# Kernel optimization log

Hardware: AMD Instinct MI355X
Metric: run time of the kernel (lower is better)

The kernel has to match this reference:

```python
import jax, jax.numpy as jnp
import numpy as np

N_NODES = 50000
N_EDGES = 800000
EDGE_DIM = 64
HID = 64


def setup_inputs() -> dict:
    key = jax.random.key(0)
    ks = jax.random.split(key, 8)
    hidden_atom_emb = jax.random.normal(ks[0], (N_NODES, HID), dtype=jnp.float32)
    edge_emb = jax.random.normal(ks[1], (N_EDGES, EDGE_DIM), dtype=jnp.float32)
    edge_list = jax.random.randint(ks[2], (N_EDGES, 2), 0, N_NODES, dtype=jnp.int64)
    # filter MLP params (xavier-uniform-like scaling)
    lim1 = float(np.sqrt(6.0 / (EDGE_DIM + HID)))
    W1 = jax.random.uniform(ks[3], (EDGE_DIM, HID), minval=-lim1, maxval=lim1, dtype=jnp.float32)
    b1 = jnp.zeros((HID,), dtype=jnp.float32)
    lim2 = float(np.sqrt(6.0 / (HID + HID)))
    W2 = jax.random.uniform(ks[4], (HID, HID), minval=-lim2, maxval=lim2, dtype=jnp.float32)
    b2 = jnp.zeros((HID,), dtype=jnp.float32)
    lim3 = 1.414 * float(np.sqrt(6.0 / (HID + 1)))
    linear_coef = jax.random.uniform(ks[5], (HID, 1), minval=-lim3, maxval=lim3, dtype=jnp.float32)
    return {
        'hidden_atom_emb': hidden_atom_emb,
        'edge_emb': edge_emb,
        'W1': W1, 'b1': b1, 'W2': W2, 'b2': b2,
        'linear_coef': linear_coef,
        'edge_list': edge_list,
    }


def reference(hidden_atom_emb, edge_emb, W1, b1, W2, b2, linear_coef, edge_list):
    # filter-generating MLP: Linear + tanh, Linear
    hidden_edge_emb = jnp.tanh(edge_emb @ W1 + b1) @ W2 + b2            # [E, H]
    # gather neighbor (source) embeddings and apply continuous filter
    msg = hidden_atom_emb[edge_list[:, 1]] * hidden_edge_emb           # [E, H]
    # unnormalized edge attention (scalar per edge)
    attn = jnp.exp(msg @ linear_coef)                                   # [E, 1]
    dest = edge_list[:, 0]
    n = hidden_atom_emb.shape[0]
    # scatter-sum over neighbors (dim=1 of the sparse [N,N,H] tensors)
    num = jax.ops.segment_sum(msg * attn, dest, num_segments=n)         # [N, H]
    den = jax.ops.segment_sum(jnp.broadcast_to(attn, msg.shape), dest, num_segments=n)  # [N, H]
    return jnp.where(den > 0, num / den, num)
```

## Files before the change

kernel.cpp:

```cpp
#include <hip/hip_runtime.h>
#include <math.h>


#define TE 64
#define HID 64
#define NBLK_MLP 768

typedef __attribute__((ext_vector_type(8))) short short8;
typedef __attribute__((ext_vector_type(4))) float float4v;

__device__ __forceinline__ float fast_tanh(float x) {
    float t = __expf(2.0f * x);
    return 1.0f - 2.0f * __builtin_amdgcn_rcpf(t + 1.0f);
}

__device__ __forceinline__ void split_bf16(float x, unsigned short& hi,
                                           unsigned short& lo) {
    unsigned b = __float_as_uint(x);
    hi = (unsigned short)(b >> 16);
    float hf = __uint_as_float(b & 0xffff0000u);
    lo = (unsigned short)(__float_as_uint(x - hf) >> 16);
}

__device__ __forceinline__ void split8(const float4 u0, const float4 u1,
                                       short8& h, short8& l) {
    float xv[8] = {u0.x, u0.y, u0.z, u0.w, u1.x, u1.y, u1.z, u1.w};
    #pragma unroll
    for (int j = 0; j < 8; ++j) {
        unsigned short hi, lo;
        split_bf16(xv[j], hi, lo);
        h[j] = (short)hi; l[j] = (short)lo;
    }
}

__device__ __forceinline__ void bar_lgkm() {
    asm volatile("s_waitcnt lgkmcnt(0)" ::: "memory");
    __builtin_amdgcn_sched_barrier(0);
    __builtin_amdgcn_s_barrier();
    __builtin_amdgcn_sched_barrier(0);
}

__device__ __forceinline__ void tile_scan(int2 pr, int lane, int w, int q,
    int& M_head, int& M_sidx, int& M_d, int& M_nseg,
    int* M_seg, int* M_src)
{
    int d = pr.x, s = pr.y;
    int dprev = __shfl_up(d, 1);
    M_head = (lane == 0 || dprev != d) ? 1 : 0;
    int sv = M_head;
    #pragma unroll
    for (int m = 1; m < 64; m <<= 1) {
        int y = __shfl_up(sv, m);
        if (lane >= m) sv += y;
    }
    M_sidx = sv - 1;
    M_d = d;
    M_nseg = __shfl(sv, 63);
    #pragma unroll
    for (int r = 0; r < 4; ++r) {
        int el = w * 16 + q * 4 + r;
        M_seg[r] = __shfl(M_sidx, el);
        M_src[r] = __shfl(s, el);
    }
}

__global__ __launch_bounds__(256) void hist_pack(
    const int2* __restrict__ edge_list, int* __restrict__ cursor, int E,
    const float* __restrict__ W1, const float* __restrict__ W2,
    unsigned short* __restrict__ wpack,
    float4* __restrict__ out4, int n4)
{
    int i = blockIdx.x * 256 + threadIdx.x;
    if (i < E) atomicAdd(&cursor[edge_list[i].x], 1);
    if (i < n4) out4[i] = (float4){0.f, 0.f, 0.f, 0.f};
    if (i < 4096) {
        int idx = i;
        int k = idx >> 6, f = idx & 63;
        int nt = f >> 4, n = f & 15, ks = k >> 5, q = (k >> 3) & 3, j = k & 7;
        int fi = (((nt * 2 + ks) * 4 + q) * 16 + n) * 8 + j;
        unsigned short hi, lo;
        split_bf16(W1[idx], hi, lo);
        wpack[fi] = hi; wpack[4096 + fi] = lo;
        split_bf16(W2[idx], hi, lo);
        wpack[8192 + fi] = hi; wpack[12288 + fi] = lo;
    }
}

__global__ __launch_bounds__(1024) void scan_single(int* __restrict__ a, int N)
{
    __shared__ int wsum[16];
    const int t = threadIdx.x, lane = t & 63, wv = t >> 6;
    int running = 0;
    const int niter = (N + 4095) / 4096;
    for (int c = 0; c < niter; ++c) {
        int base = (c * 1024 + t) * 4;
        int x0 = 0, x1 = 0, x2 = 0, x3 = 0;
        if (base + 3 < N) {
            int4 v = *(const int4*)&a[base];
            x0 = v.x; x1 = v.y; x2 = v.z; x3 = v.w;
        } else {
            if (base     < N) x0 = a[base];
            if (base + 1 < N) x1 = a[base + 1];
            if (base + 2 < N) x2 = a[base + 2];
            if (base + 3 < N) x3 = a[base + 3];
        }
        int sum = x0 + x1 + x2 + x3;
        int v = sum;
        #pragma unroll
        for (int d = 1; d < 64; d <<= 1) {
            int y = __shfl_up(v, d);
            if (lane >= d) v += y;
        }
        if (lane == 63) wsum[wv] = v;
        __syncthreads();
        if (wv == 0 && lane < 16) {
            int s2 = wsum[lane];
            #pragma unroll
            for (int d = 1; d < 16; d <<= 1) {
                int y = __shfl_up(s2, d);
                if (lane >= d) s2 += y;
            }
            wsum[lane] = s2;
        }
        __syncthreads();
        int excl = running + v - sum + (wv ? wsum[wv - 1] : 0);
        if (base     < N) a[base]     = excl;
        if (base + 1 < N) a[base + 1] = excl + x0;
        if (base + 2 < N) a[base + 2] = excl + x0 + x1;
        if (base + 3 < N) a[base + 3] = excl + x0 + x1 + x2;
        running += wsum[15];
        __syncthreads();
    }
}

__global__ __launch_bounds__(256) void perm_kernel(
    const int2* __restrict__ edge_list, int* __restrict__ cursor,
    int* __restrict__ perm, int E)
{
    int i = blockIdx.x * blockDim.x + threadIdx.x;
    if (i < E) {
        int d = edge_list[i].x;
        int p = atomicAdd(&cursor[d], 1);
        perm[p] = i;
    }
}


__global__ __launch_bounds__(256, 3) void edge_mlp_sorted(
    const float* __restrict__ atom,
    const float* __restrict__ edge_emb,
    const unsigned short* __restrict__ wpack,
    const float* __restrict__ b1,
    const float* __restrict__ b2,
    const float* __restrict__ coef,
    const int*   __restrict__ edge_list,
    const int*   __restrict__ perm,
    float* __restrict__ num,
    float* __restrict__ den,
    int E)
{
    __shared__ __align__(16) unsigned char SH[49152];
    __shared__ float denacc[TE];
    __shared__ int   segdest[TE];

    unsigned short* B1 = (unsigned short*)SH;
    unsigned short* B2 = (unsigned short*)(SH + 16384);
    float* H1  = (float*)(SH + 32768);
    float* ACC = H1;

    const int t    = threadIdx.x;
    const int w    = t >> 6;
    const int lane = t & 63;
    const int q    = lane >> 4;
    const int n    = lane & 15;
    const int ntiles = (E + TE - 1) / TE;
    const int stride = gridDim.x;

    {
        const uint4* wp = (const uint4*)wpack;
        uint4* shw = (uint4*)SH;
        #pragma unroll
        for (int i = 0; i < 8; ++i)
            shw[t + 256 * i] = wp[t + 256 * i];
    }
    float b1v[4], b2v[4], cfv[4];
    #pragma unroll
    for (int nt = 0; nt < 4; ++nt) {
        b1v[nt] = b1[nt * 16 + n];
        b2v[nt] = b2[nt * 16 + n];
        cfv[nt] = coef[nt * 16 + n];
    }
    {
        float4 z4 = {0.f, 0.f, 0.f, 0.f};
        float4* az = (float4*)ACC;
        #pragma unroll
        for (int i = 0; i < 4; ++i) az[t + 256 * i] = z4;
        if (t < TE) denacc[t] = 0.f;
    }
    __syncthreads();

    int tt = blockIdx.x;
    int m_head, m_sidx, m_d, m_nseg, m_seg[4], m_src[4];
    int pdnd = -1;
    int pA = 0;
    float4 rA0, rA1, rA2, rA3;
    {
        int eg = tt * TE + lane; if (eg >= E) eg = E - 1;
        int pc = perm[eg];
        int2 pr = ((const int2*)edge_list)[pc];
        int pid = __shfl(pc, w * 16 + n);
        const float* ep = edge_emb + (size_t)pid * HID;
        rA0 = *(const float4*)(ep + q * 8);
        rA1 = *(const float4*)(ep + q * 8 + 4);
        rA2 = *(const float4*)(ep + 32 + q * 8);
        rA3 = *(const float4*)(ep + 36 + q * 8);
        int eb = tt * TE;
        if (lane == 0 && eb > 0)       pdnd = edge_list[2 * perm[eb - 1]];
        if (lane == 63 && eb + TE < E) pdnd = edge_list[2 * perm[eb + TE]];
        tile_scan(pr, lane, w, q, m_head, m_sidx, m_d, m_nseg, m_seg, m_src);
        if (tt + stride < ntiles) {
            int eg2 = (tt + stride) * TE + lane; if (eg2 >= E) eg2 = E - 1;
            pA = perm[eg2];
        }
    }

    for (; tt < ntiles; tt += stride) {
        const int eb = tt * TE;
        const bool hn = (tt + stride) < ntiles;

        float av[4][4];
        #pragma unroll
        for (int r = 0; r < 4; ++r) {
            const float* ap = atom + (size_t)m_src[r] * HID + n;
            #pragma unroll
            for (int nt = 0; nt < 4; ++nt) av[r][nt] = ap[nt * 16];
        }

        int2 pr_n = make_int2(0, 0);
        float4 rN0 = {0,0,0,0}, rN1 = {0,0,0,0}, rN2 = {0,0,0,0}, rN3 = {0,0,0,0};
        int pB = 0, pdnd_n = -1;
        if (hn) {
            pr_n = ((const int2*)edge_list)[pA];
            int pid2 = __shfl(pA, w * 16 + n);
            const float* ep2 = edge_emb + (size_t)pid2 * HID;
            rN0 = *(const float4*)(ep2 + q * 8);
            rN1 = *(const float4*)(ep2 + q * 8 + 4);
            rN2 = *(const float4*)(ep2 + 32 + q * 8);
            rN3 = *(const float4*)(ep2 + 36 + q * 8);
            int ebn = (tt + stride) * TE;
            if (lane == 0 && ebn > 0)       pdnd_n = edge_list[2 * perm[ebn - 1]];
            if (lane == 63 && ebn + TE < E) pdnd_n = edge_list[2 * perm[ebn + TE]];
            if (tt + 2 * stride < ntiles) {
                int eg3 = (tt + 2 * stride) * TE + lane; if (eg3 >= E) eg3 = E - 1;
                pB = perm[eg3];
            }
        }

        short8 a1h[2], a1l[2];
        split8(rA0, rA1, a1h[0], a1l[0]);
        split8(rA2, rA3, a1h[1], a1l[1]);
        float4v c1[4];
        #pragma unroll
        for (int i = 0; i < 4; ++i) c1[i] = (float4v){0.f, 0.f, 0.f, 0.f};
        #pragma unroll
        for (int nt = 0; nt < 4; ++nt) {
            #pragma unroll
            for (int ks = 0; ks < 2; ++ks) {
                int cb = (nt * 2 + ks) * 64 + lane;
                short8 bh = *(const short8*)&B1[cb * 8];
                short8 bl = *(const short8*)&B1[4096 + cb * 8];
                c1[nt] = __builtin_amdgcn_mfma_f32_16x16x32_bf16(a1h[ks], bh, c1[nt], 0, 0, 0);
                c1[nt] = __builtin_amdgcn_mfma_f32_16x16x32_bf16(a1h[ks], bl, c1[nt], 0, 0, 0);
                c1[nt] = __builtin_amdgcn_mfma_f32_16x16x32_bf16(a1l[ks], bh, c1[nt], 0, 0, 0);
            }
        }

        int nm_head = 0, nm_sidx = 0, nm_d = 0, nm_nseg = 0;
        int nm_seg[4] = {0,0,0,0}, nm_src[4] = {0,0,0,0};
        if (hn)
            tile_scan(pr_n, lane, w, q, nm_head, nm_sidx, nm_d, nm_nseg,
                      nm_seg, nm_src);

        float* h1w = H1 + w * 1024;
        #pragma unroll
        for (int nt = 0; nt < 4; ++nt) {
            int f = nt * 16 + n;
            #pragma unroll
            for (int r = 0; r < 4; ++r) {
                int m = q * 4 + r;
                h1w[m * 64 + (f ^ ((m & 7) << 3))] = fast_tanh(c1[nt][r] + b1v[nt]);
            }
        }
        asm volatile("s_waitcnt lgkmcnt(0)" ::: "memory");
        __builtin_amdgcn_sched_barrier(0);

        short8 a2h[2], a2l[2];
        {
            int m = n;
            #pragma unroll
            for (int ks2 = 0; ks2 < 2; ++ks2) {
                int F0 = (ks2 * 32 + q * 8) ^ ((m & 7) << 3);
                const float* sp = h1w + m * 64 + F0;
                float4 u0 = *(const float4*)&sp[0];
                float4 u1 = *(const float4*)&sp[4];
                split8(u0, u1, a2h[ks2], a2l[ks2]);
            }
        }
        {
            float4 z4 = {0.f, 0.f, 0.f, 0.f};
            float* zp = h1w + lane * 16;
            #pragma unroll
            for (int i = 0; i < 4; ++i) *(float4*)(zp + 4 * i) = z4;
        }

        float4v c2[4];
        #pragma unroll
        for (int i = 0; i < 4; ++i) c2[i] = (float4v){0.f, 0.f, 0.f, 0.f};
        #pragma unroll
        for (int nt = 0; nt < 4; ++nt) {
            #pragma unroll
            for (int ks = 0; ks < 2; ++ks) {
                int cb = (nt * 2 + ks) * 64 + lane;
                short8 bh = *(const short8*)&B2[cb * 8];
                short8 bl = *(const short8*)&B2[4096 + cb * 8];
                c2[nt] = __builtin_amdgcn_mfma_f32_16x16x32_bf16(a2h[ks], bh, c2[nt], 0, 0, 0);
                c2[nt] = __builtin_amdgcn_mfma_f32_16x16x32_bf16(a2h[ks], bl, c2[nt], 0, 0, 0);
                c2[nt] = __builtin_amdgcn_mfma_f32_16x16x32_bf16(a2l[ks], bh, c2[nt], 0, 0, 0);
            }
        }

        float msg[4][4], partial[4], at[4];
        #pragma unroll
        for (int r = 0; r < 4; ++r) {
            float p = 0.f;
            #pragma unroll
            for (int nt = 0; nt < 4; ++nt) {
                float hv = c2[nt][r] + b2v[nt];
                msg[r][nt] = av[r][nt] * hv;
                p = fmaf(msg[r][nt], cfv[nt], p);
            }
            partial[r] = p;
        }
        #pragma unroll
        for (int m = 1; m < 16; m <<= 1) {
            #pragma unroll
            for (int r = 0; r < 4; ++r)
                partial[r] += __shfl_xor(partial[r], m);
        }
        #pragma unroll
        for (int r = 0; r < 4; ++r) {
            int eg = eb + w * 16 + q * 4 + r;
            at[r] = (eg < E) ? __expf(partial[r]) : 0.f;
        }

        bar_lgkm();

        if (m_head) segdest[m_sidx] = m_d;

        {
            int curseg = m_seg[0];
            float acc0 = msg[0][0] * at[0], acc1 = msg[0][1] * at[0];
            float acc2 = msg[0][2] * at[0], acc3 = msg[0][3] * at[0];
            float rd = at[0];
            #pragma unroll
            for (int r = 1; r < 4; ++r) {
                if (m_seg[r] == curseg) {
                    acc0 = fmaf(msg[r][0], at[r], acc0);
                    acc1 = fmaf(msg[r][1], at[r], acc1);
                    acc2 = fmaf(msg[r][2], at[r], acc2);
                    acc3 = fmaf(msg[r][3], at[r], acc3);
                    rd += at[r];
                } else {
                    float* p = &ACC[curseg * 64 + n];
                    atomicAdd(p + 0,  acc0); atomicAdd(p + 16, acc1);
                    atomicAdd(p + 32, acc2); atomicAdd(p + 48, acc3);
                    if (n == 0) atomicAdd(&denacc[curseg], rd);
                    curseg = m_seg[r];
                    acc0 = msg[r][0] * at[r]; acc1 = msg[r][1] * at[r];
                    acc2 = msg[r][2] * at[r]; acc3 = msg[r][3] * at[r];
                    rd = at[r];
                }
            }
            float* p = &ACC[curseg * 64 + n];
            atomicAdd(p + 0,  acc0); atomicAdd(p + 16, acc1);
            atomicAdd(p + 32, acc2); atomicAdd(p + 48, acc3);
            if (n == 0) atomicAdd(&denacc[curseg], rd);
        }

        bar_lgkm();

        {
            int prevd = __shfl(pdnd, 0);
            int nextd = __shfl(pdnd, 63);
            int sg = t >> 2;
            int qq = t & 3;
            if (sg < m_nseg) {
                int d2 = segdest[sg];
                bool bnd = (sg == 0 && d2 == prevd) ||
                           (sg == m_nseg - 1 && d2 == nextd);
                float* np = num + (size_t)d2 * HID + qq * 16;
                const float* sp = &ACC[sg * 64 + qq * 16];
                if (bnd) {
                    #pragma unroll
                    for (int j = 0; j < 16; ++j) atomicAdd(np + j, sp[j]);
                    if (qq == 0) { atomicAdd(&den[d2], denacc[sg]); denacc[sg] = 0.f; }
                } else {
                    #pragma unroll
                    for (int j = 0; j < 4; ++j)
                        ((float4*)np)[j] = *(const float4*)(sp + 4 * j);
                    if (qq == 0) { den[d2] = denacc[sg]; denacc[sg] = 0.f; }
                }
            }
        }

        bar_lgkm();

        if (hn) {
            m_head = nm_head; m_sidx = nm_sidx; m_d = nm_d; m_nseg = nm_nseg;
            #pragma unroll
            for (int r = 0; r < 4; ++r) { m_seg[r] = nm_seg[r]; m_src[r] = nm_src[r]; }
            pdnd = pdnd_n;
            rA0 = rN0; rA1 = rN1; rA2 = rN2; rA3 = rN3;
            pA = pB;
        }
    }
}

__global__ __launch_bounds__(256) void finalize_kernel(
    float* __restrict__ out, const float* __restrict__ den, int n16)
{
    int i = blockIdx.x * blockDim.x + threadIdx.x;
    if (i >= n16) return;
    float d = den[i >> 4];
    if (d > 0.f) {
        float4* p = (float4*)out + i;
        float4 v = *p;
        float r = 1.0f / d;
        v.x *= r; v.y *= r; v.z *= r; v.w *= r;
        *p = v;
    }
}

extern "C" void kernel_launch(void* const* d_in, const int* in_sizes, int n_in,
                              void* d_out, int out_size, void* d_ws, size_t ws_size,
                              hipStream_t stream) {
    const float* atom      = (const float*)d_in[0];
    const float* edge_emb  = (const float*)d_in[1];
    const float* W1        = (const float*)d_in[2];
    const float* b1        = (const float*)d_in[3];
    const float* W2        = (const float*)d_in[4];
    const float* b2        = (const float*)d_in[5];
    const float* coef      = (const float*)d_in[6];
    const int*   edge_list = (const int*)d_in[7];

    const int N = in_sizes[0] / HID;
    const int E = in_sizes[1] / HID;

    float* den       = (float*)d_ws;
    int*   cursor    = (int*)d_ws + N;
    int*   perm      = (int*)d_ws + 2 * N + 64;
    unsigned short* wpack = (unsigned short*)((int*)d_ws + 2 * N + 64 + E);

    hipMemsetAsync(d_ws, 0, (size_t)(2 * N) * sizeof(int), stream);

    int n4   = N * (HID / 4);
    int eblk = (E + 255) / 256;
    int ghp  = eblk > (n4 + 255) / 256 ? eblk : (n4 + 255) / 256;
    hist_pack<<<ghp, 256, 0, stream>>>((const int2*)edge_list, cursor, E,
                                       W1, W2, wpack, (float4*)d_out, n4);
    scan_single<<<1, 1024, 0, stream>>>(cursor, N);
    perm_kernel<<<eblk, 256, 0, stream>>>((const int2*)edge_list, cursor, perm, E);

    int ntl  = (E + TE - 1) / TE;
    int nblk = ntl < NBLK_MLP ? ntl : NBLK_MLP;
    edge_mlp_sorted<<<nblk, 256, 0, stream>>>(
        atom, edge_emb, wpack, b1, b2, coef, edge_list, perm,
        (float*)d_out, den, E);

    finalize_kernel<<<(n4 + 255) / 256, 256, 0, stream>>>((float*)d_out, den, n4);
}
```

Measured before the change: 526.1 us.

## Pair two edge tiles per 512-thread block and parallelize the degree scan

The edge MLP kernel now runs 512 threads per block as two 4-wave groups. Each group handles its own 64-edge tile and keeps its own accumulation region, while both share the weight copy in LDS, which cuts weight staging per tile and changes occupancy. The single-block prefix scan over node degrees becomes a three-kernel multi-block scan: per-block scan, scan of block sums, then add-back. The tighter launch bounds (512,4) may cap VGPRs low enough to cause spills, and the scan adds two more kernel launches.

After: 660.6 us. +25.6%, slower.

```diff
diff --git a/kernel.cpp b/kernel.cpp
--- a/kernel.cpp
+++ b/kernel.cpp
@@ -4,7 +4,7 @@
 
 #define TE 64
 #define HID 64
-#define NBLK_MLP 768
+#define NBLK_MLP 512
 
 typedef __attribute__((ext_vector_type(8))) short short8;
 typedef __attribute__((ext_vector_type(4))) float float4v;
@@ -40,7 +40,7 @@
     __builtin_amdgcn_sched_barrier(0);
 }
 
-__device__ __forceinline__ void tile_scan(int2 pr, int lane, int w, int q,
+__device__ __forceinline__ void tile_scan(int2 pr, int lane, int wl, int q,
     int& M_head, int& M_sidx, int& M_d, int& M_nseg,
     int* M_seg, int* M_src)
 {
@@ -58,7 +58,7 @@
     M_nseg = __shfl(sv, 63);
     #pragma unroll
     for (int r = 0; r < 4; ++r) {
-        int el = w * 16 + q * 4 + r;
+        int el = wl * 16 + q * 4 + r;
         M_seg[r] = __shfl(M_sidx, el);
         M_src[r] = __shfl(s, el);
     }
@@ -86,51 +86,55 @@
     }
 }
 
-__global__ __launch_bounds__(1024) void scan_single(int* __restrict__ a, int N)
+__global__ __launch_bounds__(1024) void scanA_kernel(
+    int* __restrict__ a, int* __restrict__ blocksums, int N)
 {
     __shared__ int wsum[16];
-    const int t = threadIdx.x, lane = t & 63, wv = t >> 6;
-    int running = 0;
-    const int niter = (N + 4095) / 4096;
-    for (int c = 0; c < niter; ++c) {
-        int base = (c * 1024 + t) * 4;
-        int x0 = 0, x1 = 0, x2 = 0, x3 = 0;
-        if (base + 3 < N) {
-            int4 v = *(const int4*)&a[base];
-            x0 = v.x; x1 = v.y; x2 = v.z; x3 = v.w;
-        } else {
-            if (base     < N) x0 = a[base];
-            if (base + 1 < N) x1 = a[base + 1];
-            if (base + 2 < N) x2 = a[base + 2];
-            if (base + 3 < N) x3 = a[base + 3];
-        }
-        int sum = x0 + x1 + x2 + x3;
-        int v = sum;
-        #pragma unroll
-        for (int d = 1; d < 64; d <<= 1) {
-            int y = __shfl_up(v, d);
-            if (lane >= d) v += y;
-        }
-        if (lane == 63) wsum[wv] = v;
-        __syncthreads();
-        if (wv == 0 && lane < 16) {
-            int s2 = wsum[lane];
-            #pragma unroll
-            for (int d = 1; d < 16; d <<= 1) {
-                int y = __shfl_up(s2, d);
-                if (lane >= d) s2 += y;
-            }
-            wsum[lane] = s2;
-        }
-        __syncthreads();
-        int excl = running + v - sum + (wv ? wsum[wv - 1] : 0);
-        if (base     < N) a[base]     = excl;
-        if (base + 1 < N) a[base + 1] = excl + x0;
-        if (base + 2 < N) a[base + 2] = excl + x0 + x1;
-        if (base + 3 < N) a[base + 3] = excl + x0 + x1 + x2;
-        running += wsum[15];
-        __syncthreads();
-    }
+    const int t = threadIdx.x;
+    const int lane = t & 63, wv = t >> 6;
+    int i = blockIdx.x * 1024 + t;
+    int x = (i < N) ? a[i] : 0;
+    int v = x;
+    #pragma unroll
+    for (int d = 1; d < 64; d <<= 1) {
+        int y = __shfl_up(v, d);
+        if (lane >= d) v += y;
+    }
+    if (lane == 63) wsum[wv] = v;
+    __syncthreads();
+    if (wv == 0 && lane < 16) {
+        int s = wsum[lane];
+        #pragma unroll
+        for (int d = 1; d < 16; d <<= 1) {
+            int y = __shfl_up(s, d);
+            if (lane >= d) s += y;
+        }
+        wsum[lane] = s;
+    }
+    __syncthreads();
+    int incl = v + ((wv == 0) ? 0 : wsum[wv - 1]);
+    if (i < N) a[i] = incl - x;
+    if (t == 1023) blocksums[blockIdx.x] = incl;
+}
+
+__global__ __launch_bounds__(64) void scanB_kernel(int* __restrict__ bs, int nb)
+{
+    int lane = threadIdx.x;
+    int x = (lane < nb) ? bs[lane] : 0;
+    int v = x;
+    #pragma unroll
+    for (int d = 1; d < 64; d <<= 1) {
+        int y = __shfl_up(v, d);
+        if (lane >= d) v += y;
+    }
+    if (lane < nb) bs[lane] = v - x;
+}
+
+__global__ __launch_bounds__(1024) void scanC_kernel(
+    int* __restrict__ a, const int* __restrict__ blocksums, int N)
+{
+    int i = blockIdx.x * 1024 + threadIdx.x;
+    if (i < N) a[i] += blocksums[blockIdx.x];
 }
 
 __global__ __launch_bounds__(256) void perm_kernel(
@@ -146,7 +150,7 @@
 }
 
 
-__global__ __launch_bounds__(256, 3) void edge_mlp_sorted(
+__global__ __launch_bounds__(512, 4) void edge_mlp_sorted(
     const float* __restrict__ atom,
     const float* __restrict__ edge_emb,
     const unsigned short* __restrict__ wpack,
@@ -159,9 +163,9 @@
     float* __restrict__ den,
     int E)
 {
-    __shared__ __align__(16) unsigned char SH[49152];
-    __shared__ float denacc[TE];
-    __shared__ int   segdest[TE];
+    __shared__ __align__(16) unsigned char SH[65536];
+    __shared__ float denacc[128];
+    __shared__ int   segdest[128];
 
     unsigned short* B1 = (unsigned short*)SH;
     unsigned short* B2 = (unsigned short*)(SH + 16384);
@@ -170,18 +174,21 @@
 
     const int t    = threadIdx.x;
     const int w    = t >> 6;
+    const int g    = w >> 2;
+    const int wl   = w & 3;
     const int lane = t & 63;
     const int q    = lane >> 4;
     const int n    = lane & 15;
-    const int ntiles = (E + TE - 1) / TE;
+    const int NT     = (E + TE - 1) / TE;
+    const int ntiles = (NT + 1) / 2;
     const int stride = gridDim.x;
 
     {
         const uint4* wp = (const uint4*)wpack;
         uint4* shw = (uint4*)SH;
         #pragma unroll
-        for (int i = 0; i < 8; ++i)
-            shw[t + 256 * i] = wp[t + 256 * i];
+        for (int i = 0; i < 4; ++i)
+            shw[t + 512 * i] = wp[t + 512 * i];
     }
     float b1v[4], b2v[4], cfv[4];
     #pragma unroll
@@ -194,8 +201,8 @@
         float4 z4 = {0.f, 0.f, 0.f, 0.f};
         float4* az = (float4*)ACC;
         #pragma unroll
-        for (int i = 0; i < 4; ++i) az[t + 256 * i] = z4;
-        if (t < TE) denacc[t] = 0.f;
+        for (int i = 0; i < 4; ++i) az[t + 512 * i] = z4;
+        if (t < 128) denacc[t] = 0.f;
     }
     __syncthreads();
 
@@ -205,28 +212,32 @@
     int pA = 0;
     float4 rA0, rA1, rA2, rA3;
     {
-        int eg = tt * TE + lane; if (eg >= E) eg = E - 1;
+        int st  = 2 * tt + g;
+        int ebg = st * TE;
+        int eg = ebg + lane; if (eg >= E) eg = E - 1;
         int pc = perm[eg];
         int2 pr = ((const int2*)edge_list)[pc];
-        int pid = __shfl(pc, w * 16 + n);
+        int pid = __shfl(pc, wl * 16 + n);
         const float* ep = edge_emb + (size_t)pid * HID;
         rA0 = *(const float4*)(ep + q * 8);
         rA1 = *(const float4*)(ep + q * 8 + 4);
         rA2 = *(const float4*)(ep + 32 + q * 8);
         rA3 = *(const float4*)(ep + 36 + q * 8);
-        int eb = tt * TE;
-        if (lane == 0 && eb > 0)       pdnd = edge_list[2 * perm[eb - 1]];
-        if (lane == 63 && eb + TE < E) pdnd = edge_list[2 * perm[eb + TE]];
-        tile_scan(pr, lane, w, q, m_head, m_sidx, m_d, m_nseg, m_seg, m_src);
+        if (lane == 0 && ebg > 0)       pdnd = edge_list[2 * perm[ebg - 1]];
+        if (lane == 63 && ebg + TE < E) pdnd = edge_list[2 * perm[ebg + TE]];
+        tile_scan(pr, lane, wl, q, m_head, m_sidx, m_d, m_nseg, m_seg, m_src);
         if (tt + stride < ntiles) {
-            int eg2 = (tt + stride) * TE + lane; if (eg2 >= E) eg2 = E - 1;
+            int eg2 = (2 * (tt + stride) + g) * TE + lane;
+            if (eg2 >= E) eg2 = E - 1;
             pA = perm[eg2];
         }
     }
 
     for (; tt < ntiles; tt += stride) {
-        const int eb = tt * TE;
-        const bool hn = (tt + stride) < ntiles;
+        const int st  = 2 * tt + g;
+        const int ebg = st * TE;
+        const bool stv = st < NT;
+        const bool hn  = (tt + stride) < ntiles;
 
         float av[4][4];
         #pragma unroll
@@ -241,17 +252,18 @@
         int pB = 0, pdnd_n = -1;
         if (hn) {
             pr_n = ((const int2*)edge_list)[pA];
-            int pid2 = __shfl(pA, w * 16 + n);
+            int pid2 = __shfl(pA, wl * 16 + n);
             const float* ep2 = edge_emb + (size_t)pid2 * HID;
             rN0 = *(const float4*)(ep2 + q * 8);
             rN1 = *(const float4*)(ep2 + q * 8 + 4);
             rN2 = *(const float4*)(ep2 + 32 + q * 8);
             rN3 = *(const float4*)(ep2 + 36 + q * 8);
-            int ebn = (tt + stride) * TE;
+            int ebn = (2 * (tt + stride) + g) * TE;
             if (lane == 0 && ebn > 0)       pdnd_n = edge_list[2 * perm[ebn - 1]];
             if (lane == 63 && ebn + TE < E) pdnd_n = edge_list[2 * perm[ebn + TE]];
             if (tt + 2 * stride < ntiles) {
-                int eg3 = (tt + 2 * stride) * TE + lane; if (eg3 >= E) eg3 = E - 1;
+                int eg3 = (2 * (tt + 2 * stride) + g) * TE + lane;
+                if (eg3 >= E) eg3 = E - 1;
                 pB = perm[eg3];
             }
         }
@@ -278,7 +290,7 @@
         int nm_head = 0, nm_sidx = 0, nm_d = 0, nm_nseg = 0;
         int nm_seg[4] = {0,0,0,0}, nm_src[4] = {0,0,0,0};
         if (hn)
-            tile_scan(pr_n, lane, w, q, nm_head, nm_sidx, nm_d, nm_nseg,
+            tile_scan(pr_n, lane, wl, q, nm_head, nm_sidx, nm_d, nm_nseg,
                       nm_seg, nm_src);
 
         float* h1w = H1 + w * 1024;
@@ -349,13 +361,13 @@
         }
         #pragma unroll
         for (int r = 0; r < 4; ++r) {
-            int eg = eb + w * 16 + q * 4 + r;
+            int eg = ebg + wl * 16 + q * 4 + r;
             at[r] = (eg < E) ? __expf(partial[r]) : 0.f;
         }
 
         bar_lgkm();
 
-        if (m_head) segdest[m_sidx] = m_d;
+        if (m_head) segdest[64 * g + m_sidx] = m_d;
 
         {
             int curseg = m_seg[0];
@@ -371,20 +383,20 @@
                     acc3 = fmaf(msg[r][3], at[r], acc3);
                     rd += at[r];
                 } else {
-                    float* p = &ACC[curseg * 64 + n];
+                    float* p = &ACC[(64 * g + curseg) * 64 + n];
                     atomicAdd(p + 0,  acc0); atomicAdd(p + 16, acc1);
                     atomicAdd(p + 32, acc2); atomicAdd(p + 48, acc3);
-                    if (n == 0) atomicAdd(&denacc[curseg], rd);
+                    if (n == 0) atomicAdd(&denacc[64 * g + curseg], rd);
                     curseg = m_seg[r];
                     acc0 = msg[r][0] * at[r]; acc1 = msg[r][1] * at[r];
                     acc2 = msg[r][2] * at[r]; acc3 = msg[r][3] * at[r];
                     rd = at[r];
                 }
             }
-            float* p = &ACC[curseg * 64 + n];
+            float* p = &ACC[(64 * g + curseg) * 64 + n];
             atomicAdd(p + 0,  acc0); atomicAdd(p + 16, acc1);
             atomicAdd(p + 32, acc2); atomicAdd(p + 48, acc3);
-            if (n == 0) atomicAdd(&denacc[curseg], rd);
+            if (n == 0) atomicAdd(&denacc[64 * g + curseg], rd);
         }
 
         bar_lgkm();
@@ -392,12 +404,13 @@
         {
             int prevd = __shfl(pdnd, 0);
             int nextd = __shfl(pdnd, 63);
-            int sg = t >> 2;
-            int qq = t & 3;
-            if (sg < m_nseg) {
+            int sg  = t >> 2;
+            int sgl = sg & 63;
+            int qq  = t & 3;
+            if (stv && sgl < m_nseg) {
                 int d2 = segdest[sg];
-                bool bnd = (sg == 0 && d2 == prevd) ||
-                           (sg == m_nseg - 1 && d2 == nextd);
+                bool bnd = (sgl == 0 && d2 == prevd) ||
+                           (sgl == m_nseg - 1 && d2 == nextd);
                 float* np = num + (size_t)d2 * HID + qq * 16;
                 const float* sp = &ACC[sg * 64 + qq * 16];
                 if (bnd) {
@@ -458,6 +471,7 @@
 
     float* den       = (float*)d_ws;
     int*   cursor    = (int*)d_ws + N;
+    int*   blocksums = (int*)d_ws + 2 * N;
     int*   perm      = (int*)d_ws + 2 * N + 64;
     unsigned short* wpack = (unsigned short*)((int*)d_ws + 2 * N + 64 + E);
 
@@ -465,15 +479,18 @@
 
     int n4   = N * (HID / 4);
     int eblk = (E + 255) / 256;
+    int nb   = (N + 1023) / 1024;
     int ghp  = eblk > (n4 + 255) / 256 ? eblk : (n4 + 255) / 256;
     hist_pack<<<ghp, 256, 0, stream>>>((const int2*)edge_list, cursor, E,
                                        W1, W2, wpack, (float4*)d_out, n4);
-    scan_single<<<1, 1024, 0, stream>>>(cursor, N);
+    scanA_kernel<<<nb, 1024, 0, stream>>>(cursor, blocksums, N);
+    scanB_kernel<<<1, 64, 0, stream>>>(blocksums, nb);
+    scanC_kernel<<<nb, 1024, 0, stream>>>(cursor, blocksums, N);
     perm_kernel<<<eblk, 256, 0, stream>>>((const int2*)edge_list, cursor, perm, E);
 
-    int ntl  = (E + TE - 1) / TE;
-    int nblk = ntl < NBLK_MLP ? ntl : NBLK_MLP;
-    edge_mlp_sorted<<<nblk, 256, 0, stream>>>(
+    int npairs = ((E + TE - 1) / TE + 1) / 2;
+    int nblk   = npairs < NBLK_MLP ? npairs : NBLK_MLP;
+    edge_mlp_sorted<<<nblk, 512, 0, stream>>>(
         atom, edge_emb, wpack, b1, b2, coef, edge_list, perm,
         (float*)d_out, den, E);
 
```

## Fuse histogram, scan and permutation into one persistent kernel with grid barriers

Applied to the files above, without the earlier changes.

Replaces the three preprocessing kernels (histogram+pack, single-block scan, permutation) with one persistent kernel of 512 blocks that uses software grid barriers between phases. The scan becomes a parallel multi-block scan with a block-sums pass instead of a serial single-block loop over all nodes. This removes two launch gaps and the slow single-block scan, in exchange for four spin-wait grid barriers. It also relies on all 512 blocks being co-resident, otherwise the barriers deadlock.

Result: slower. 781.5 us (+48.5%).

```diff
diff --git a/kernel.cpp b/kernel.cpp
--- a/kernel.cpp
+++ b/kernel.cpp
@@ -5,6 +5,7 @@
 #define TE 64
 #define HID 64
 #define NBLK_MLP 768
+#define NBLK_AUX 512
 
 typedef __attribute__((ext_vector_type(8))) short short8;
 typedef __attribute__((ext_vector_type(4))) float float4v;
@@ -38,6 +39,24 @@
     __builtin_amdgcn_sched_barrier(0);
     __builtin_amdgcn_s_barrier();
     __builtin_amdgcn_sched_barrier(0);
+}
+
+__device__ __forceinline__ void gbar(int* cnt, int* gen, int nblk) {
+    __syncthreads();
+    if (threadIdx.x == 0) {
+        __threadfence();
+        int g = __hip_atomic_load(gen, __ATOMIC_RELAXED, __HIP_MEMORY_SCOPE_AGENT);
+        int a = __hip_atomic_fetch_add(cnt, 1, __ATOMIC_ACQ_REL, __HIP_MEMORY_SCOPE_AGENT);
+        if (a == nblk - 1) {
+            __hip_atomic_store(cnt, 0, __ATOMIC_RELAXED, __HIP_MEMORY_SCOPE_AGENT);
+            __hip_atomic_store(gen, g + 1, __ATOMIC_RELEASE, __HIP_MEMORY_SCOPE_AGENT);
+        } else {
+            while (__hip_atomic_load(gen, __ATOMIC_ACQUIRE, __HIP_MEMORY_SCOPE_AGENT) == g)
+                __builtin_amdgcn_s_sleep(2);
+        }
+        __threadfence();
+    }
+    __syncthreads();
 }
 
 __device__ __forceinline__ void tile_scan(int2 pr, int lane, int w, int q,
@@ -64,17 +83,25 @@
     }
 }
 
-__global__ __launch_bounds__(256) void hist_pack(
-    const int2* __restrict__ edge_list, int* __restrict__ cursor, int E,
+__global__ __launch_bounds__(256) void aux_mega(
+    const int2* __restrict__ edge_list, int* __restrict__ cursor,
+    int* __restrict__ blocksums, int* __restrict__ bar,
+    int* __restrict__ perm, int E, int N,
     const float* __restrict__ W1, const float* __restrict__ W2,
     unsigned short* __restrict__ wpack,
     float4* __restrict__ out4, int n4)
 {
-    int i = blockIdx.x * 256 + threadIdx.x;
-    if (i < E) atomicAdd(&cursor[edge_list[i].x], 1);
-    if (i < n4) out4[i] = (float4){0.f, 0.f, 0.f, 0.f};
-    if (i < 4096) {
-        int idx = i;
+    __shared__ int wsumI[4];
+    const int t = threadIdx.x;
+    const int lane = t & 63, wv = t >> 6;
+    const int G = gridDim.x * 256;
+    const int gid = blockIdx.x * 256 + t;
+    const int nblk = gridDim.x;
+
+    for (int i = gid; i < n4; i += G) out4[i] = (float4){0.f, 0.f, 0.f, 0.f};
+    for (int i = gid; i < E; i += G) atomicAdd(&cursor[edge_list[i].x], 1);
+    if (gid < 4096) {
+        int idx = gid;
         int k = idx >> 6, f = idx & 63;
         int nt = f >> 4, n = f & 15, ks = k >> 5, q = (k >> 3) & 3, j = k & 7;
         int fi = (((nt * 2 + ks) * 4 + q) * 16 + n) * 8 + j;
@@ -84,61 +111,64 @@
         split_bf16(W2[idx], hi, lo);
         wpack[8192 + fi] = hi; wpack[12288 + fi] = lo;
     }
-}
-
-__global__ __launch_bounds__(1024) void scan_single(int* __restrict__ a, int N)
-{
-    __shared__ int wsum[16];
-    const int t = threadIdx.x, lane = t & 63, wv = t >> 6;
-    int running = 0;
-    const int niter = (N + 4095) / 4096;
-    for (int c = 0; c < niter; ++c) {
-        int base = (c * 1024 + t) * 4;
+    gbar(bar, bar + 1, nblk);
+
+    const int nchunks = (N + 1023) >> 10;
+    if ((int)blockIdx.x < nchunks) {
+        int base = blockIdx.x * 1024 + t * 4;
         int x0 = 0, x1 = 0, x2 = 0, x3 = 0;
         if (base + 3 < N) {
-            int4 v = *(const int4*)&a[base];
-            x0 = v.x; x1 = v.y; x2 = v.z; x3 = v.w;
+            int4 v4 = *(const int4*)&cursor[base];
+            x0 = v4.x; x1 = v4.y; x2 = v4.z; x3 = v4.w;
         } else {
-            if (base     < N) x0 = a[base];
-            if (base + 1 < N) x1 = a[base + 1];
-            if (base + 2 < N) x2 = a[base + 2];
-            if (base + 3 < N) x3 = a[base + 3];
-        }
-        int sum = x0 + x1 + x2 + x3;
-        int v = sum;
-        #pragma unroll
-        for (int d = 1; d < 64; d <<= 1) {
-            int y = __shfl_up(v, d);
-            if (lane >= d) v += y;
-        }
-        if (lane == 63) wsum[wv] = v;
+            if (base     < N) x0 = cursor[base];
+            if (base + 1 < N) x1 = cursor[base + 1];
+            if (base + 2 < N) x2 = cursor[base + 2];
+            if (base + 3 < N) x3 = cursor[base + 3];
+        }
+        int s = x0 + x1 + x2 + x3;
+        int v = s;
+        #pragma unroll
+        for (int dd = 1; dd < 64; dd <<= 1) {
+            int y = __shfl_up(v, dd);
+            if (lane >= dd) v += y;
+        }
+        if (lane == 63) wsumI[wv] = v;
         __syncthreads();
-        if (wv == 0 && lane < 16) {
-            int s2 = wsum[lane];
-            #pragma unroll
-            for (int d = 1; d < 16; d <<= 1) {
-                int y = __shfl_up(s2, d);
-                if (lane >= d) s2 += y;
-            }
-            wsum[lane] = s2;
-        }
-        __syncthreads();
-        int excl = running + v - sum + (wv ? wsum[wv - 1] : 0);
-        if (base     < N) a[base]     = excl;
-        if (base + 1 < N) a[base + 1] = excl + x0;
-        if (base + 2 < N) a[base + 2] = excl + x0 + x1;
-        if (base + 3 < N) a[base + 3] = excl + x0 + x1 + x2;
-        running += wsum[15];
-        __syncthreads();
-    }
-}
-
-__global__ __launch_bounds__(256) void perm_kernel(
-    const int2* __restrict__ edge_list, int* __restrict__ cursor,
-    int* __restrict__ perm, int E)
-{
-    int i = blockIdx.x * blockDim.x + threadIdx.x;
-    if (i < E) {
+        int w0 = wsumI[0], w1 = wsumI[1], w2 = wsumI[2], w3 = wsumI[3];
+        int woff = (wv == 0) ? 0 : (wv == 1) ? w0 : (wv == 2) ? w0 + w1
+                                                             : w0 + w1 + w2;
+        int excl = woff + v - s;
+        if (base     < N) cursor[base]     = excl;
+        if (base + 1 < N) cursor[base + 1] = excl + x0;
+        if (base + 2 < N) cursor[base + 2] = excl + x0 + x1;
+        if (base + 3 < N) cursor[base + 3] = excl + x0 + x1 + x2;
+        if (t == 0) blocksums[blockIdx.x] = w0 + w1 + w2 + w3;
+    }
+    gbar(bar, bar + 1, nblk);
+
+    if (blockIdx.x == 0 && wv == 0) {
+        int x = (lane < nchunks) ? blocksums[lane] : 0;
+        int v = x;
+        #pragma unroll
+        for (int dd = 1; dd < 64; dd <<= 1) {
+            int y = __shfl_up(v, dd);
+            if (lane >= dd) v += y;
+        }
+        if (lane < nchunks) blocksums[lane] = v - x;
+    }
+    gbar(bar, bar + 1, nblk);
+
+    if ((int)blockIdx.x < nchunks) {
+        int add = blocksums[blockIdx.x];
+        int base = blockIdx.x * 1024 + t * 4;
+        #pragma unroll
+        for (int j = 0; j < 4; ++j)
+            if (base + j < N) cursor[base + j] += add;
+    }
+    gbar(bar, bar + 1, nblk);
+
+    for (int i = gid; i < E; i += G) {
         int d = edge_list[i].x;
         int p = atomicAdd(&cursor[d], 1);
         perm[p] = i;
@@ -458,18 +488,17 @@
 
     float* den       = (float*)d_ws;
     int*   cursor    = (int*)d_ws + N;
-    int*   perm      = (int*)d_ws + 2 * N + 64;
-    unsigned short* wpack = (unsigned short*)((int*)d_ws + 2 * N + 64 + E);
-
-    hipMemsetAsync(d_ws, 0, (size_t)(2 * N) * sizeof(int), stream);
-
-    int n4   = N * (HID / 4);
-    int eblk = (E + 255) / 256;
-    int ghp  = eblk > (n4 + 255) / 256 ? eblk : (n4 + 255) / 256;
-    hist_pack<<<ghp, 256, 0, stream>>>((const int2*)edge_list, cursor, E,
-                                       W1, W2, wpack, (float4*)d_out, n4);
-    scan_single<<<1, 1024, 0, stream>>>(cursor, N);
-    perm_kernel<<<eblk, 256, 0, stream>>>((const int2*)edge_list, cursor, perm, E);
+    int*   blocksums = (int*)d_ws + 2 * N;
+    int*   bar       = (int*)d_ws + 2 * N + 64;
+    int*   perm      = (int*)d_ws + 2 * N + 128;
+    unsigned short* wpack = (unsigned short*)((int*)d_ws + 2 * N + 128 + E);
+
+    hipMemsetAsync(d_ws, 0, (size_t)(2 * N + 128) * sizeof(int), stream);
+
+    int n4 = N * (HID / 4);
+    aux_mega<<<NBLK_AUX, 256, 0, stream>>>(
+        (const int2*)edge_list, cursor, blocksums, bar, perm, E, N,
+        W1, W2, wpack, (float4*)d_out, n4);
 
     int ntl  = (E + TE - 1) / TE;
     int nblk = ntl < NBLK_MLP ? ntl : NBLK_MLP;
```

## Parallelize offset scan across blocks and record per-edge rank to drop second atomic pass

Applied to the files above, without the earlier changes.

The single-block serial scan over node counts is replaced by a three-kernel multi-block scan: per-block scan, a scan of the block sums, then adding the offsets back. The histogram pass now saves each edge's atomic return value as a 16-bit rank, so the permutation pass computes its slot from offset plus rank instead of doing a second atomic. This removes a serial single-workgroup bottleneck and contended atomics, at the cost of two extra launches and an extra E-sized rank buffer. The scan-of-blocksums uses one wave, so it assumes at most 64 blocks (N ≤ 65536), and ranks assume per-node degree fits in 16 bits.

After: 470.8 us. 10.5% less time.

```diff
diff --git a/kernel.cpp b/kernel.cpp
--- a/kernel.cpp
+++ b/kernel.cpp
@@ -65,13 +65,17 @@
 }
 
 __global__ __launch_bounds__(256) void hist_pack(
-    const int2* __restrict__ edge_list, int* __restrict__ cursor, int E,
+    const int2* __restrict__ edge_list, int* __restrict__ cursor,
+    unsigned short* __restrict__ rank, int E,
     const float* __restrict__ W1, const float* __restrict__ W2,
     unsigned short* __restrict__ wpack,
     float4* __restrict__ out4, int n4)
 {
     int i = blockIdx.x * 256 + threadIdx.x;
-    if (i < E) atomicAdd(&cursor[edge_list[i].x], 1);
+    if (i < E) {
+        int r = atomicAdd(&cursor[edge_list[i].x], 1);
+        rank[i] = (unsigned short)r;
+    }
     if (i < n4) out4[i] = (float4){0.f, 0.f, 0.f, 0.f};
     if (i < 4096) {
         int idx = i;
@@ -86,61 +90,65 @@
     }
 }
 
-__global__ __launch_bounds__(1024) void scan_single(int* __restrict__ a, int N)
+__global__ __launch_bounds__(1024) void scanA_kernel(
+    int* __restrict__ a, int* __restrict__ blocksums, int N)
 {
     __shared__ int wsum[16];
-    const int t = threadIdx.x, lane = t & 63, wv = t >> 6;
-    int running = 0;
-    const int niter = (N + 4095) / 4096;
-    for (int c = 0; c < niter; ++c) {
-        int base = (c * 1024 + t) * 4;
-        int x0 = 0, x1 = 0, x2 = 0, x3 = 0;
-        if (base + 3 < N) {
-            int4 v = *(const int4*)&a[base];
-            x0 = v.x; x1 = v.y; x2 = v.z; x3 = v.w;
-        } else {
-            if (base     < N) x0 = a[base];
-            if (base + 1 < N) x1 = a[base + 1];
-            if (base + 2 < N) x2 = a[base + 2];
-            if (base + 3 < N) x3 = a[base + 3];
-        }
-        int sum = x0 + x1 + x2 + x3;
-        int v = sum;
-        #pragma unroll
-        for (int d = 1; d < 64; d <<= 1) {
-            int y = __shfl_up(v, d);
-            if (lane >= d) v += y;
-        }
-        if (lane == 63) wsum[wv] = v;
-        __syncthreads();
-        if (wv == 0 && lane < 16) {
-            int s2 = wsum[lane];
-            #pragma unroll
-            for (int d = 1; d < 16; d <<= 1) {
-                int y = __shfl_up(s2, d);
-                if (lane >= d) s2 += y;
-            }
-            wsum[lane] = s2;
-        }
-        __syncthreads();
-        int excl = running + v - sum + (wv ? wsum[wv - 1] : 0);
-        if (base     < N) a[base]     = excl;
-        if (base + 1 < N) a[base + 1] = excl + x0;
-        if (base + 2 < N) a[base + 2] = excl + x0 + x1;
-        if (base + 3 < N) a[base + 3] = excl + x0 + x1 + x2;
-        running += wsum[15];
-        __syncthreads();
-    }
+    const int t = threadIdx.x;
+    const int lane = t & 63, wv = t >> 6;
+    int i = blockIdx.x * 1024 + t;
+    int x = (i < N) ? a[i] : 0;
+    int v = x;
+    #pragma unroll
+    for (int d = 1; d < 64; d <<= 1) {
+        int y = __shfl_up(v, d);
+        if (lane >= d) v += y;
+    }
+    if (lane == 63) wsum[wv] = v;
+    __syncthreads();
+    if (wv == 0 && lane < 16) {
+        int s = wsum[lane];
+        #pragma unroll
+        for (int d = 1; d < 16; d <<= 1) {
+            int y = __shfl_up(s, d);
+            if (lane >= d) s += y;
+        }
+        wsum[lane] = s;
+    }
+    __syncthreads();
+    int incl = v + ((wv == 0) ? 0 : wsum[wv - 1]);
+    if (i < N) a[i] = incl - x;
+    if (t == 1023) blocksums[blockIdx.x] = incl;
+}
+
+__global__ __launch_bounds__(64) void scanB_kernel(int* __restrict__ bs, int nb)
+{
+    int lane = threadIdx.x;
+    int x = (lane < nb) ? bs[lane] : 0;
+    int v = x;
+    #pragma unroll
+    for (int d = 1; d < 64; d <<= 1) {
+        int y = __shfl_up(v, d);
+        if (lane >= d) v += y;
+    }
+    if (lane < nb) bs[lane] = v - x;
+}
+
+__global__ __launch_bounds__(1024) void scanC_kernel(
+    int* __restrict__ a, const int* __restrict__ blocksums, int N)
+{
+    int i = blockIdx.x * 1024 + threadIdx.x;
+    if (i < N) a[i] += blocksums[blockIdx.x];
 }
 
 __global__ __launch_bounds__(256) void perm_kernel(
-    const int2* __restrict__ edge_list, int* __restrict__ cursor,
-    int* __restrict__ perm, int E)
+    const int2* __restrict__ edge_list, const int* __restrict__ cursor,
+    const unsigned short* __restrict__ rank, int* __restrict__ perm, int E)
 {
     int i = blockIdx.x * blockDim.x + threadIdx.x;
     if (i < E) {
         int d = edge_list[i].x;
-        int p = atomicAdd(&cursor[d], 1);
+        int p = cursor[d] + (int)rank[i];
         perm[p] = i;
     }
 }
@@ -458,18 +466,24 @@
 
     float* den       = (float*)d_ws;
     int*   cursor    = (int*)d_ws + N;
+    int*   blocksums = (int*)d_ws + 2 * N;
     int*   perm      = (int*)d_ws + 2 * N + 64;
-    unsigned short* wpack = (unsigned short*)((int*)d_ws + 2 * N + 64 + E);
+    unsigned short* rank  = (unsigned short*)((int*)d_ws + 2 * N + 64 + E);
+    unsigned short* wpack = rank + E;
 
     hipMemsetAsync(d_ws, 0, (size_t)(2 * N) * sizeof(int), stream);
 
     int n4   = N * (HID / 4);
     int eblk = (E + 255) / 256;
+    int nb   = (N + 1023) / 1024;
     int ghp  = eblk > (n4 + 255) / 256 ? eblk : (n4 + 255) / 256;
-    hist_pack<<<ghp, 256, 0, stream>>>((const int2*)edge_list, cursor, E,
+    hist_pack<<<ghp, 256, 0, stream>>>((const int2*)edge_list, cursor, rank, E,
                                        W1, W2, wpack, (float4*)d_out, n4);
-    scan_single<<<1, 1024, 0, stream>>>(cursor, N);
-    perm_kernel<<<eblk, 256, 0, stream>>>((const int2*)edge_list, cursor, perm, E);
+    scanA_kernel<<<nb, 1024, 0, stream>>>(cursor, blocksums, N);
+    scanB_kernel<<<1, 64, 0, stream>>>(blocksums, nb);
+    scanC_kernel<<<nb, 1024, 0, stream>>>(cursor, blocksums, N);
+    perm_kernel<<<eblk, 256, 0, stream>>>((const int2*)edge_list, cursor, rank,
+                                          perm, E);
 
     int ntl  = (E + TE - 1) / TE;
     int nblk = ntl < NBLK_MLP ? ntl : NBLK_MLP;
```
